# Kernel tuning notes

Hardware: AMD Instinct MI355X
Metric: run time of the kernel (lower is better)

Reference implementation:

```python
import jax, jax.numpy as jnp
import numpy as np
import math

DIM = 128
HEAD = 4
RANK = 32
HEAD_DIM = DIM // HEAD
B, T, N, F = 2, 128, 1024, 128  # t == f == dim required by the original module
EXPAND = 4
EPS = 1e-6


def setup_inputs() -> dict:
    key = jax.random.key(0)
    ks = jax.random.split(key, 12)
    s = 0.02
    return {
        "x": jax.random.normal(ks[0], (B, T, N, F), jnp.float32),
        "norm_w": jnp.ones((DIM,), jnp.float32),
        "q_w": jax.random.normal(ks[1], (DIM, DIM), jnp.float32) * s,   # (out,in)
        "q_b": jnp.zeros((DIM,), jnp.float32),
        "key_p": jax.random.normal(ks[2], (RANK, HEAD, HEAD_DIM), jnp.float32),
        "v_w": jax.random.normal(ks[3], (DIM, DIM), jnp.float32) * s,
        "v_b": jnp.zeros((DIM,), jnp.float32),
        "alpha": jnp.full((HEAD, 1), math.log(9.0), jnp.float32),
        "beta": jnp.full((HEAD, 1), math.log(0.01), jnp.float32),
        "w1": jax.random.normal(ks[4], (EXPAND * DIM, DIM), jnp.float32) * s,
        "b1": jnp.zeros((EXPAND * DIM,), jnp.float32),
        "w2": jax.random.normal(ks[5], (EXPAND * DIM, DIM), jnp.float32) * s,
        "b2": jnp.zeros((EXPAND * DIM,), jnp.float32),
        "w3": jax.random.normal(ks[6], (DIM, EXPAND * DIM), jnp.float32) * s,
        "b3": jnp.zeros((DIM,), jnp.float32),
    }


def _rmsnorm(x, w):
    # NOTE: original reduces over axis 1 (the t axis), weight broadcasts on last axis
    var = jnp.mean(x * x, axis=1, keepdims=True)
    return w * (x * jax.lax.rsqrt(var + EPS))


def _attention(x, q_w, q_b, key_p, v_w, v_b, alpha, beta):
    b, t, n, f = x.shape
    q = (jnp.einsum('btnf,of->btno', x, q_w) + q_b).reshape(b, t, n, HEAD, HEAD_DIM)
    attn = jnp.einsum('btnhd,rhd->btnhr', q, key_p) / (HEAD_DIM ** 0.5)
    xv = (jnp.einsum('btnf,of->btno', x, v_w) + v_b).reshape(b, t, n, HEAD, HEAD_DIM)
    # softmax over rank, aggregate values into landmarks
    v = jnp.einsum('btnhr,btnhd->btrhd', jax.nn.softmax(attn, axis=-1), xv)
    # softmax over node axis (axis=-3 of btnhr), scatter landmarks back to nodes
    v = jnp.einsum('btnhr,btrhd->btnhd', jax.nn.softmax(attn, axis=-3), v)
    v = jax.nn.sigmoid(alpha) * xv + jax.nn.sigmoid(beta) * v
    return v.reshape(b, t, n, f)


def _conv1x1(x, w, b):
    # Conv2d kernel_size=1 on (B, C=t, H=n, W=f)
    return jnp.einsum('oc,bcnf->bonf', w, x) + b[None, :, None, None]


def _ffn(x, w1, b1, w2, b2, w3, b3):
    h = jax.nn.silu(_conv1x1(x, w1, b1)) * _conv1x1(x, w2, b2)
    return _conv1x1(h, w3, b3)  # dropout is identity in eval mode


def reference(x, norm_w, q_w, q_b, key_p, v_w, v_b, alpha, beta,
              w1, b1, w2, b2, w3, b3):
    x = _attention(_rmsnorm(x, norm_w), q_w, q_b, key_p, v_w, v_b, alpha, beta) + x
    x = _ffn(_rmsnorm(x, norm_w), w1, b1, w2, b2, w3, b3) + x
    return x
```

## Files before the change

kernel.cpp:

```cpp
#include <hip/hip_runtime.h>

#define DEV static __device__ __forceinline__

constexpr int Bc = 2, Tc = 128, Nc = 1024, Fc = 128, Hc = 4, Rc = 32, Dc = 32;
constexpr int NF  = Nc * Fc;
constexpr int TOK = Bc * Tc * Nc;
constexpr float EPSc = 1e-6f;
constexpr float RSD  = 0.17677669529663687f;

typedef __bf16 bf16x8 __attribute__((ext_vector_type(8)));
typedef float  f32x16 __attribute__((ext_vector_type(16)));
typedef unsigned short us8 __attribute__((ext_vector_type(8)));
typedef unsigned short us4 __attribute__((ext_vector_type(4)));

DEV unsigned short f2bu(float f) {
    unsigned u = __builtin_bit_cast(unsigned, f);
    u += 0x7fffu + ((u >> 16) & 1u);
    return (unsigned short)(u >> 16);
}
DEV float bu2f(unsigned short s) {
    return __builtin_bit_cast(float, ((unsigned)s) << 16);
}
DEV float sigmoidf_(float z) { return 1.f / (1.f + __expf(-z)); }
DEV f32x16 zero16() { f32x16 z;
#pragma unroll
    for (int i = 0; i < 16; i++) z[i] = 0.f;
    return z; }

__global__ void k_prep(const float* __restrict__ x, float* __restrict__ inv,
                       const float* __restrict__ q_w, const float* __restrict__ q_b,
                       const float* __restrict__ key_p, const float* __restrict__ v_b,
                       const float* __restrict__ v_w,
                       unsigned short* __restrict__ Wcat, float* __restrict__ bias,
                       const float* __restrict__ w1, const float* __restrict__ w2,
                       const float* __restrict__ w3, unsigned short* __restrict__ wbf)
{
    __shared__ float sqw[32][128];
    __shared__ float skp[32][32];
    const int blk = blockIdx.x, tid = threadIdx.x;
    if (blk < 1024) {
        int j = blk * 256 + tid;
        int b = j >> 17;
        int p = j & (NF - 1);
        const float* px = x + (size_t)b * Tc * NF + p;
        float s = 0.f;
#pragma unroll 8
        for (int t = 0; t < Tc; ++t) { float v = px[(size_t)t * NF]; s = fmaf(v, v, s); }
        inv[j] = rsqrtf(s * (1.f / Tc) + EPSc);
        return;
    }
    if (blk < 1028) {
        int h = blk - 1024;
        for (int i = tid; i < 4096; i += 256) {
            int d = i >> 7, c = i & 127;
            sqw[d][c] = q_w[(size_t)(h * 32 + d) * 128 + c];
        }
        for (int i = tid; i < 1024; i += 256) {
            int r = i >> 5, d = i & 31;
            skp[r][d] = key_p[(size_t)(r * 4 + h) * 32 + d] * RSD;
        }
        __syncthreads();
        int r = tid >> 3;
        int c0 = (tid & 7) * 16;
        for (int cc = 0; cc < 16; ++cc) {
            int c = c0 + cc;
            float s = 0.f;
#pragma unroll
            for (int d = 0; d < 32; ++d) s = fmaf(sqw[d][c], skp[r][d], s);
            Wcat[(size_t)(h * 32 + r) * 128 + c] = f2bu(s);
        }
        if (tid < 32) {
            float s = 0.f;
#pragma unroll
            for (int d = 0; d < 32; ++d) s = fmaf(q_b[h * 32 + d], skp[tid][d], s);
            bias[h * 32 + tid] = s;
        }
        if (h == 0 && tid >= 64 && tid < 192) bias[128 + tid - 64] = v_b[tid - 64];
        return;
    }
    if (blk < 1092) {
        int i = (blk - 1028) * 256 + tid;
        Wcat[16384 + i] = f2bu(v_w[i]);
        return;
    }
    {
        int i = (blk - 1092) * 256 + tid;
        float v;
        if (i < 65536)       v = w1[i];
        else if (i < 131072) v = w2[i - 65536];
        else                 v = w3[i - 131072];
        wbf[i] = f2bu(v);
    }
}

__global__ __launch_bounds__(256, 4) void k_projm(
    const float* __restrict__ x, const float* __restrict__ inv1, const float* __restrict__ nw,
    const unsigned short* __restrict__ Wcat, const float* __restrict__ bias,
    unsigned short* __restrict__ Lb, unsigned short* __restrict__ XVb)
{
    const int tid = threadIdx.x, lane = tid & 63, wv = tid >> 6;
    const int lr = lane & 31, lhi = lane >> 5;
    const int tokb = blockIdx.x * 128 + wv * 32;
    const int tok = tokb + lr;
    const int b = tok >> 17, n = tok & 1023;
    const float* px = x + (size_t)tok * 128;
    const float* pi = inv1 + (size_t)b * NF + n * 128;

    bf16x8 af[8];
#pragma unroll
    for (int s = 0; s < 8; ++s) {
        const int c0 = s * 16 + lhi * 8;
        float4 xa = *(const float4*)(px + c0);
        float4 xb = *(const float4*)(px + c0 + 4);
        float4 ia = *(const float4*)(pi + c0);
        float4 ib = *(const float4*)(pi + c0 + 4);
        float4 na = *(const float4*)(nw + c0);
        float4 nb = *(const float4*)(nw + c0 + 4);
        bf16x8 v;
        v[0] = (__bf16)(xa.x * ia.x * na.x);
        v[1] = (__bf16)(xa.y * ia.y * na.y);
        v[2] = (__bf16)(xa.z * ia.z * na.z);
        v[3] = (__bf16)(xa.w * ia.w * na.w);
        v[4] = (__bf16)(xb.x * ib.x * nb.x);
        v[5] = (__bf16)(xb.y * ib.y * nb.y);
        v[6] = (__bf16)(xb.z * ib.z * nb.z);
        v[7] = (__bf16)(xb.w * ib.w * nb.w);
        af[s] = v;
    }

#pragma unroll
    for (int ot = 0; ot < 8; ++ot) {
        const unsigned short* pw = Wcat + (size_t)(ot * 32 + lr) * 128 + lhi * 8;
        f32x16 acc = zero16();
#pragma unroll
        for (int s = 0; s < 8; ++s) {
            bf16x8 bw = *(const bf16x8*)(pw + s * 16);
            acc = __builtin_amdgcn_mfma_f32_32x32x16_bf16(af[s], bw, acc, 0, 0, 0);
        }
        const int o = ot * 32 + lr;
        const float bv = bias[o];
        unsigned short* dst = (ot < 4) ? Lb : XVb;
        const int oo = (ot < 4) ? o : o - 128;
#pragma unroll
        for (int r = 0; r < 16; ++r) {
            const int trow = tokb + (r & 3) + 8 * (r >> 2) + 4 * lhi;
            dst[(size_t)trow * 128 + oo] = f2bu(acc[r] + bv);
        }
    }
}

__global__ __launch_bounds__(256, 4) void k_land(
    const unsigned short* __restrict__ Lb, const unsigned short* __restrict__ XVb,
    float* __restrict__ VL, float* __restrict__ M2, float* __restrict__ S2)
{
    __shared__ float sL [64][34];
    __shared__ float sXV[64][36];
    __shared__ float redm[32][8];
    __shared__ float reds[32][8];
    int tid = threadIdx.x;
    int blk = blockIdx.x;
    int h = blk & 3; int bt = blk >> 2;
    size_t base = (size_t)bt * Nc * 128 + h * 32;
    const int li = tid >> 2, c8 = (tid & 3) * 8;
    const int r_st = tid & 31, stripe = tid >> 5;
    const int ti = tid >> 2, sub = tid & 3;
    const int r_acc = tid >> 3, d0 = (tid & 7) * 4;
    float m_st = -1e30f, s_st = 0.f;
    float a0 = 0, a1 = 0, a2 = 0, a3 = 0;
    for (int n0 = 0; n0 < Nc; n0 += 64) {
        {
            size_t g = base + (size_t)(n0 + li) * 128 + c8;
            us8 vL = *(const us8*)(Lb + g);
            us8 vX = *(const us8*)(XVb + g);
#pragma unroll
            for (int j = 0; j < 8; ++j) {
                sL [li][c8 + j] = bu2f(vL[j]);
                sXV[li][c8 + j] = bu2f(vX[j]);
            }
        }
        __syncthreads();
#pragma unroll
        for (int i8 = 0; i8 < 8; ++i8) {
            float v = sL[stripe * 8 + i8][r_st];
            float mn = fmaxf(m_st, v);
            s_st = s_st * __expf(m_st - mn) + __expf(v - mn);
            m_st = mn;
        }
        float e[8];
        float mx = -1e30f;
#pragma unroll
        for (int j = 0; j < 8; ++j) mx = fmaxf(mx, sL[ti][sub * 8 + j]);
        mx = fmaxf(mx, __shfl_xor(mx, 1));
        mx = fmaxf(mx, __shfl_xor(mx, 2));
        float sm = 0.f;
#pragma unroll
        for (int j = 0; j < 8; ++j) { e[j] = __expf(sL[ti][sub * 8 + j] - mx); sm += e[j]; }
        sm += __shfl_xor(sm, 1);
        sm += __shfl_xor(sm, 2);
        float iv = 1.f / sm;
        __syncthreads();
#pragma unroll
        for (int j = 0; j < 8; ++j) sL[ti][sub * 8 + j] = e[j] * iv;
        __syncthreads();
#pragma unroll 2
        for (int i = 0; i < 64; ++i) {
            float p = sL[i][r_acc];
            float4 v = *(const float4*)&sXV[i][d0];
            a0 = fmaf(p, v.x, a0); a1 = fmaf(p, v.y, a1);
            a2 = fmaf(p, v.z, a2); a3 = fmaf(p, v.w, a3);
        }
        __syncthreads();
    }
    redm[r_st][stripe] = m_st;
    reds[r_st][stripe] = s_st;
    __syncthreads();
    if (tid < 32) {
        float m = -1e30f;
#pragma unroll
        for (int k = 0; k < 8; ++k) m = fmaxf(m, redm[tid][k]);
        float s = 0.f;
#pragma unroll
        for (int k = 0; k < 8; ++k) s += reds[tid][k] * __expf(redm[tid][k] - m);
        M2[blk * 32 + tid] = m;
        S2[blk * 32 + tid] = s;
    }
    *(float4*)&VL[((size_t)blk * 32 + r_acc) * 32 + d0] = make_float4(a0, a1, a2, a3);
}

__global__ __launch_bounds__(256) void k_out1(
    const float* __restrict__ x,
    const unsigned short* __restrict__ Lb, const unsigned short* __restrict__ XVb,
    const float* __restrict__ VL, const float* __restrict__ M2, const float* __restrict__ S2,
    const float* __restrict__ alpha, const float* __restrict__ beta,
    unsigned short* __restrict__ X2b)
{
    __shared__ float sVL[128][32];
    __shared__ float sP[8][128];
    __shared__ float sM[128], sSi[128], sAB[8];
    int tid = threadIdx.x;
    int tk00 = blockIdx.x * 32;
    int bt = tk00 >> 10;
    for (int k = tid; k < 4096; k += 256) sVL[k >> 5][k & 31] = VL[(size_t)bt * 4096 + k];
    if (tid < 128) { sM[tid] = M2[bt * 128 + tid]; sSi[tid] = 1.f / S2[bt * 128 + tid]; }
    if (tid < 8)   sAB[tid] = (tid < 4) ? sigmoidf_(alpha[tid]) : sigmoidf_(beta[tid - 4]);
    __syncthreads();
    const int ti = tid >> 5, quad = tid & 31;
    const int h = quad >> 3, d0 = (quad & 7) * 4;
    const int hr0 = h * 32;
    const int f4 = (tid & 31) * 4;
    const float sa = sAB[h], sb = sAB[4 + h];
    for (int tg = 0; tg < 4; ++tg) {
        const int tk0 = tk00 + tg * 8;
        {
            us4 lv = *(const us4*)&Lb[(size_t)(tk0 + ti) * 128 + f4];
#pragma unroll
            for (int j = 0; j < 4; ++j)
                sP[ti][f4 + j] = __expf(bu2f(lv[j]) - sM[f4 + j]) * sSi[f4 + j];
        }
        __syncthreads();
        float a0 = 0, a1 = 0, a2 = 0, a3 = 0;
#pragma unroll 4
        for (int r = 0; r < 32; ++r) {
            float p = sP[ti][hr0 + r];
            float4 v = *(const float4*)&sVL[hr0 + r][d0];
            a0 = fmaf(p, v.x, a0); a1 = fmaf(p, v.y, a1);
            a2 = fmaf(p, v.z, a2); a3 = fmaf(p, v.w, a3);
        }
        size_t gi = (size_t)(tk0 + ti) * 128 + quad * 4;
        ushort4 xv4 = *(const ushort4*)&XVb[gi];
        float o0 = fmaf(sb, a0, fmaf(sa, bu2f(xv4.x), x[gi + 0]));
        float o1 = fmaf(sb, a1, fmaf(sa, bu2f(xv4.y), x[gi + 1]));
        float o2 = fmaf(sb, a2, fmaf(sa, bu2f(xv4.z), x[gi + 2]));
        float o3 = fmaf(sb, a3, fmaf(sa, bu2f(xv4.w), x[gi + 3]));
        ushort4 pk; pk.x = f2bu(o0); pk.y = f2bu(o1); pk.z = f2bu(o2); pk.w = f2bu(o3);
        *(ushort4*)&X2b[gi] = pk;
        __syncthreads();
    }
}

constexpr int XST = 132;
__global__ __launch_bounds__(256, 2) void k_ffn_mfma(
    const unsigned short* __restrict__ X2b, const float* __restrict__ nw,
    const unsigned short* __restrict__ w1b, const float* __restrict__ b1,
    const unsigned short* __restrict__ w2b, const float* __restrict__ b2,
    const unsigned short* __restrict__ w3b, const float* __restrict__ b3,
    float* __restrict__ out)
{
    __shared__ unsigned short smem[18432] __attribute__((aligned(16)));
    unsigned short* xstage = smem;
    unsigned short* gT     = smem;
    __shared__ float sscale[128];

    const int tid  = threadIdx.x;
    const int lane = tid & 63;
    const int wv   = tid >> 6;
    const int lr   = lane & 31;
    const int lhi  = lane >> 5;
    const int blk  = blockIdx.x;
    const int b    = blk >> 10, n = blk & 1023;

    const int mrow = (wv & 1) * 32;
    const int fh   = (wv >> 1) * 64;
    const int t0   = wv * 32;

    const unsigned short* xg = X2b + ((size_t)(b * Tc) * Nc + n) * 128;
#pragma unroll
    for (int p = 0; p < 8; ++p) {
        int i = p * 256 + tid;
        int t = i >> 4, fg = i & 15;
        us8 v = *(const us8*)(xg + (size_t)t * NF + fg * 8);
        int tt = t ^ ((fg & 7) << 3);
#pragma unroll
        for (int j = 0; j < 8; ++j) xstage[(fg * 8 + j) * XST + tt] = v[j];
    }
    __syncthreads();

    {
        int f = tid >> 1, half = tid & 1;
        float ss = 0.f;
#pragma unroll
        for (int kk = 0; kk < 16; ++kk) {
            us4 u = *(const us4*)&xstage[f * XST + half * 64 + kk * 4];
#pragma unroll
            for (int j = 0; j < 4; ++j) { float v = bu2f(u[j]); ss = fmaf(v, v, ss); }
        }
        ss += __shfl_xor(ss, 1);
        if (half == 0) sscale[f] = rsqrtf(ss * (1.f / Tc) + EPSc) * nw[f];
    }
    __syncthreads();

    bf16x8 xnf[2][8];
#pragma unroll
    for (int ft = 0; ft < 2; ++ft) {
        const int f = fh + ft * 32 + lr;
        const int swz = ((f >> 3) & 7) << 3;
        const float scale = sscale[f];
#pragma unroll
        for (int s = 0; s < 8; ++s) {
            int tb = (s * 16 + lhi * 8) ^ swz;
            us4 u0 = *(const us4*)&xstage[f * XST + tb];
            us4 u1 = *(const us4*)&xstage[f * XST + tb + 4];
            bf16x8 v;
#pragma unroll
            for (int j = 0; j < 4; ++j) {
                v[j]     = (__bf16)(bu2f(u0[j]) * scale);
                v[j + 4] = (__bf16)(bu2f(u1[j]) * scale);
            }
            xnf[ft][s] = v;
        }
    }

    f32x16 oacc[4];
#pragma unroll
    for (int c = 0; c < 4; ++c) {
        const int f = c * 32 + lr;
        const int swz = ((f >> 3) & 7) << 3;
#pragma unroll
        for (int q = 0; q < 4; ++q) {
            const int tb = t0 + 8 * q + 4 * lhi;
            us4 u = *(const us4*)&xstage[f * XST + (tb ^ swz)];
#pragma unroll
            for (int e = 0; e < 4; ++e)
                oacc[c][q * 4 + e] = bu2f(u[e]) + b3[tb + e];
        }
    }
    __syncthreads();

    const unsigned short* w1r = w1b + (size_t)(mrow + lr) * 128 + lhi * 8;
    const unsigned short* w2r = w2b + (size_t)(mrow + lr) * 128 + lhi * 8;
    const unsigned short* w3r = w3b + (size_t)(t0 + lr) * 512 + lhi * 8;

    int d = 0;
    for (int oc = 0; oc < 512; oc += 64) {
        bf16x8 a3[4];
        const unsigned short* pw3 = w3r + oc;
#pragma unroll
        for (int s = 0; s < 4; ++s) a3[s] = *(const bf16x8*)(pw3 + s * 16);

        f32x16 h1a = zero16(), h1b = zero16(), h2a = zero16(), h2b = zero16();
        const unsigned short* pw1 = w1r + (size_t)oc * 128;
        const unsigned short* pw2 = w2r + (size_t)oc * 128;
#pragma unroll
        for (int s = 0; s < 8; ++s) {
            bf16x8 a1 = *(const bf16x8*)(pw1 + s * 16);
            bf16x8 a2 = *(const bf16x8*)(pw2 + s * 16);
            h1a = __builtin_amdgcn_mfma_f32_32x32x16_bf16(a1, xnf[0][s], h1a, 0, 0, 0);
            h1b = __builtin_amdgcn_mfma_f32_32x32x16_bf16(a1, xnf[1][s], h1b, 0, 0, 0);
            h2a = __builtin_amdgcn_mfma_f32_32x32x16_bf16(a2, xnf[0][s], h2a, 0, 0, 0);
            h2b = __builtin_amdgcn_mfma_f32_32x32x16_bf16(a2, xnf[1][s], h2b, 0, 0, 0);
        }
        unsigned short* gTd = gT + d * 9216;
#pragma unroll
        for (int ft = 0; ft < 2; ++ft) {
            const int fcol = fh + ft * 32 + lr;
#pragma unroll
            for (int q = 0; q < 4; ++q) {
                ushort4 pk;
#pragma unroll
                for (int e = 0; e < 4; ++e) {
                    const int r = q * 4 + e;
                    const int orow = oc + mrow + e + 8 * q + 4 * lhi;
                    float z   = (ft ? h1b[r] : h1a[r]) + b1[orow];
                    float h2v = (ft ? h2b[r] : h2a[r]) + b2[orow];
                    float g   = z * sigmoidf_(z) * h2v;
                    unsigned short gb = f2bu(g);
                    if (e == 0) pk.x = gb; else if (e == 1) pk.y = gb;
                    else if (e == 2) pk.z = gb; else pk.w = gb;
                }
                const int o_l = mrow + 8 * q + 4 * lhi;
                *(ushort4*)&gTd[fcol * 72 + o_l] = pk;
            }
        }
        __syncthreads();
#pragma unroll
        for (int s = 0; s < 4; ++s) {
#pragma unroll
            for (int c = 0; c < 4; ++c) {
                bf16x8 bg = *(const bf16x8*)&gTd[(c * 32 + lr) * 72 + s * 16 + lhi * 8];
                oacc[c] = __builtin_amdgcn_mfma_f32_32x32x16_bf16(a3[s], bg, oacc[c], 0, 0, 0);
            }
        }
        d ^= 1;
    }

#pragma unroll
    for (int r = 0; r < 16; ++r) {
        const int t = t0 + (r & 3) + 8 * (r >> 2) + 4 * lhi;
        const size_t rowbase = ((size_t)(b * Tc + t) * Nc + n) * 128;
#pragma unroll
        for (int c = 0; c < 4; ++c) {
            out[rowbase + c * 32 + lr] = oacc[c][r];
        }
    }
}

extern "C" void kernel_launch(void* const* d_in, const int* in_sizes, int n_in,
                              void* d_out, int out_size, void* d_ws, size_t ws_size,
                              hipStream_t stream) {
    const float* x      = (const float*)d_in[0];
    const float* norm_w = (const float*)d_in[1];
    const float* q_w    = (const float*)d_in[2];
    const float* q_b    = (const float*)d_in[3];
    const float* key_p  = (const float*)d_in[4];
    const float* v_w    = (const float*)d_in[5];
    const float* v_b    = (const float*)d_in[6];
    const float* alpha  = (const float*)d_in[7];
    const float* beta   = (const float*)d_in[8];
    const float* w1     = (const float*)d_in[9];
    const float* b1     = (const float*)d_in[10];
    const float* w2     = (const float*)d_in[11];
    const float* b2     = (const float*)d_in[12];
    const float* w3     = (const float*)d_in[13];
    const float* b3     = (const float*)d_in[14];
    float* out = (float*)d_out;

    char* ws = (char*)d_ws;
    float* inv1 = (float*)ws;
    float* inv2 = inv1 + (size_t)Bc * NF;
    float* VLp  = inv2 + (size_t)Bc * NF;
    float* M2p  = VLp + (size_t)Bc * Tc * Hc * Rc * Dc;
    float* S2p  = M2p + (size_t)Bc * Tc * Hc * Rc;
    unsigned short* Lb  = (unsigned short*)(S2p + (size_t)Bc * Tc * Hc * Rc);
    unsigned short* XVb = Lb  + (size_t)TOK * 128;
    unsigned short* X2b = XVb + (size_t)TOK * 128;

    unsigned short* Wcat = (unsigned short*)VLp;
    float* bias256 = VLp + 16384;

    unsigned short* w1bf = (unsigned short*)inv2;
    unsigned short* w2bf = w1bf + 65536;
    unsigned short* w3bf = w1bf + 131072;

    k_prep    <<<1860,          256, 0, stream>>>(x, inv1, q_w, q_b, key_p, v_b, v_w,
                                                  Wcat, bias256, w1, w2, w3, w1bf);
    k_projm   <<<TOK / 128,     256, 0, stream>>>(x, inv1, norm_w, Wcat, bias256, Lb, XVb);
    k_land    <<<Bc * Tc * Hc,  256, 0, stream>>>(Lb, XVb, VLp, M2p, S2p);
    k_out1    <<<TOK / 32,      256, 0, stream>>>(x, Lb, XVb, VLp, M2p, S2p, alpha, beta, X2b);
    k_ffn_mfma<<<Bc * Nc,       256, 0, stream>>>(X2b, norm_w, w1bf, b1, w2bf, b2, w3bf, b3, out);
}
```

Before: 525.8 us.

## Fuse first RMSNorm statistics into projection kernel via per-(b,n) tiling

Removes the separate pass in k_prep that read all of x to compute the t-axis RMS scale. k_projm now assigns one block per (b,n), loads the full 128x128 t-by-f slab into swizzled shared memory, reduces over t in-block, and feeds normalized bf16 fragments to the MFMA. This saves one full read of x and the inv1 round-trip. In exchange it uses about 67KB of LDS per block, lowers occupancy to 2 blocks, and scatters output stores with a stride of Nc*128.

```diff
diff --git a/kernel.cpp b/kernel.cpp
--- a/kernel.cpp
+++ b/kernel.cpp
@@ -27,8 +27,7 @@
     for (int i = 0; i < 16; i++) z[i] = 0.f;
     return z; }
 
-__global__ void k_prep(const float* __restrict__ x, float* __restrict__ inv,
-                       const float* __restrict__ q_w, const float* __restrict__ q_b,
+__global__ void k_prep(const float* __restrict__ q_w, const float* __restrict__ q_b,
                        const float* __restrict__ key_p, const float* __restrict__ v_b,
                        const float* __restrict__ v_w,
                        unsigned short* __restrict__ Wcat, float* __restrict__ bias,
@@ -38,19 +37,8 @@
     __shared__ float sqw[32][128];
     __shared__ float skp[32][32];
     const int blk = blockIdx.x, tid = threadIdx.x;
-    if (blk < 1024) {
-        int j = blk * 256 + tid;
-        int b = j >> 17;
-        int p = j & (NF - 1);
-        const float* px = x + (size_t)b * Tc * NF + p;
-        float s = 0.f;
-#pragma unroll 8
-        for (int t = 0; t < Tc; ++t) { float v = px[(size_t)t * NF]; s = fmaf(v, v, s); }
-        inv[j] = rsqrtf(s * (1.f / Tc) + EPSc);
-        return;
-    }
-    if (blk < 1028) {
-        int h = blk - 1024;
+    if (blk < 4) {
+        int h = blk;
         for (int i = tid; i < 4096; i += 256) {
             int d = i >> 7, c = i & 127;
             sqw[d][c] = q_w[(size_t)(h * 32 + d) * 128 + c];
@@ -78,13 +66,13 @@
         if (h == 0 && tid >= 64 && tid < 192) bias[128 + tid - 64] = v_b[tid - 64];
         return;
     }
-    if (blk < 1092) {
-        int i = (blk - 1028) * 256 + tid;
+    if (blk < 68) {
+        int i = (blk - 4) * 256 + tid;
         Wcat[16384 + i] = f2bu(v_w[i]);
         return;
     }
     {
-        int i = (blk - 1092) * 256 + tid;
+        int i = (blk - 68) * 256 + tid;
         float v;
         if (i < 65536)       v = w1[i];
         else if (i < 131072) v = w2[i - 65536];
@@ -93,38 +81,58 @@
     }
 }
 
-__global__ __launch_bounds__(256, 4) void k_projm(
-    const float* __restrict__ x, const float* __restrict__ inv1, const float* __restrict__ nw,
+constexpr int XPF = 132;
+__global__ __launch_bounds__(256, 2) void k_projm(
+    const float* __restrict__ x, const float* __restrict__ nw,
     const unsigned short* __restrict__ Wcat, const float* __restrict__ bias,
     unsigned short* __restrict__ Lb, unsigned short* __restrict__ XVb)
 {
+    __shared__ float xs[128 * XPF];
+    __shared__ float sscale[128];
     const int tid = threadIdx.x, lane = tid & 63, wv = tid >> 6;
     const int lr = lane & 31, lhi = lane >> 5;
-    const int tokb = blockIdx.x * 128 + wv * 32;
-    const int tok = tokb + lr;
-    const int b = tok >> 17, n = tok & 1023;
-    const float* px = x + (size_t)tok * 128;
-    const float* pi = inv1 + (size_t)b * NF + n * 128;
+    const int blk = blockIdx.x;
+    const int b = blk >> 10, n = blk & 1023;
+
+    const float* xg = x + ((size_t)(b * Tc) * Nc + n) * 128;
+#pragma unroll
+    for (int p = 0; p < 8; ++p) {
+        int i = p * 256 + tid;
+        int t = i >> 4, cg = i & 15;
+        const float* src = xg + (size_t)t * NF + cg * 8;
+        float4 u0 = *(const float4*)src;
+        float4 u1 = *(const float4*)(src + 4);
+        int col = t ^ ((cg & 7) << 3);
+        float vv[8] = {u0.x, u0.y, u0.z, u0.w, u1.x, u1.y, u1.z, u1.w};
+#pragma unroll
+        for (int j = 0; j < 8; ++j) xs[(cg * 8 + j) * XPF + col] = vv[j];
+    }
+    __syncthreads();
+
+    {
+        int c = tid >> 1, half = tid & 1;
+        float ss = 0.f;
+#pragma unroll
+        for (int k = 0; k < 16; ++k) {
+            float4 u = *(const float4*)&xs[c * XPF + half * 64 + k * 4];
+            ss = fmaf(u.x, u.x, fmaf(u.y, u.y, fmaf(u.z, u.z, fmaf(u.w, u.w, ss))));
+        }
+        ss += __shfl_xor(ss, 1);
+        if (half == 0) sscale[c] = rsqrtf(ss * (1.f / Tc) + EPSc) * nw[c];
+    }
+    __syncthreads();
 
     bf16x8 af[8];
 #pragma unroll
     for (int s = 0; s < 8; ++s) {
-        const int c0 = s * 16 + lhi * 8;
-        float4 xa = *(const float4*)(px + c0);
-        float4 xb = *(const float4*)(px + c0 + 4);
-        float4 ia = *(const float4*)(pi + c0);
-        float4 ib = *(const float4*)(pi + c0 + 4);
-        float4 na = *(const float4*)(nw + c0);
-        float4 nb = *(const float4*)(nw + c0 + 4);
+        const int cbase = s * 16 + lhi * 8;
+        const int col = (wv * 32 + lr) ^ (((cbase >> 3) & 7) << 3);
         bf16x8 v;
-        v[0] = (__bf16)(xa.x * ia.x * na.x);
-        v[1] = (__bf16)(xa.y * ia.y * na.y);
-        v[2] = (__bf16)(xa.z * ia.z * na.z);
-        v[3] = (__bf16)(xa.w * ia.w * na.w);
-        v[4] = (__bf16)(xb.x * ib.x * nb.x);
-        v[5] = (__bf16)(xb.y * ib.y * nb.y);
-        v[6] = (__bf16)(xb.z * ib.z * nb.z);
-        v[7] = (__bf16)(xb.w * ib.w * nb.w);
+#pragma unroll
+        for (int j = 0; j < 8; ++j) {
+            const int c = cbase + j;
+            v[j] = (__bf16)(xs[c * XPF + col] * sscale[c]);
+        }
         af[s] = v;
     }
 
@@ -143,8 +151,8 @@
         const int oo = (ot < 4) ? o : o - 128;
 #pragma unroll
         for (int r = 0; r < 16; ++r) {
-            const int trow = tokb + (r & 3) + 8 * (r >> 2) + 4 * lhi;
-            dst[(size_t)trow * 128 + oo] = f2bu(acc[r] + bv);
+            const int t = wv * 32 + (r & 3) + 8 * (r >> 2) + 4 * lhi;
+            dst[((size_t)(b * Tc + t) * Nc + n) * 128 + oo] = f2bu(acc[r] + bv);
         }
     }
 }
@@ -471,9 +479,9 @@
     unsigned short* w2bf = w1bf + 65536;
     unsigned short* w3bf = w1bf + 131072;
 
-    k_prep    <<<1860,          256, 0, stream>>>(x, inv1, q_w, q_b, key_p, v_b, v_w,
+    k_prep    <<<836,           256, 0, stream>>>(q_w, q_b, key_p, v_b, v_w,
                                                   Wcat, bias256, w1, w2, w3, w1bf);
-    k_projm   <<<TOK / 128,     256, 0, stream>>>(x, inv1, norm_w, Wcat, bias256, Lb, XVb);
+    k_projm   <<<Bc * Nc,       256, 0, stream>>>(x, norm_w, Wcat, bias256, Lb, XVb);
     k_land    <<<Bc * Tc * Hc,  256, 0, stream>>>(Lb, XVb, VLp, M2p, S2p);
     k_out1    <<<TOK / 32,      256, 0, stream>>>(x, Lb, XVb, VLp, M2p, S2p, alpha, beta, X2b);
     k_ffn_mfma<<<Bc * Nc,       256, 0, stream>>>(X2b, norm_w, w1bf, b1, w2bf, b2, w3bf, b3, out);
```

Result: faster. 492.5 us (median of 3 runs) (-6.3%).
